# Kernel tuning notes

Measured on AMD Instinct MI355X. Metric: run time of the kernel, lower is better.

The kernel has to match this reference:

```python
import jax, jax.numpy as jnp
import numpy as np

N_NODES = 100000
EMB_DIM = 64
N_EDGES = 1200000
N_LAYERS = 3


def setup_inputs() -> dict:
    key = jax.random.key(0)
    k1, k2, k3 = jax.random.split(key, 3)
    embedding = jax.random.normal(k1, (N_NODES, EMB_DIM), dtype=jnp.float32)
    layer_weights = jnp.ones((N_LAYERS + 1,), dtype=jnp.float32) / (N_LAYERS + 1)
    edge_weight = jax.random.uniform(k2, (N_EDGES,), dtype=jnp.float32)
    edge_index = jax.random.randint(k3, (2, N_EDGES), 0, N_NODES, dtype=jnp.int64)
    return {"embedding": embedding, "layer_weights": layer_weights,
            "edge_weight": edge_weight, "edge_index": edge_index}


def reference(embedding, layer_weights, edge_weight, edge_index):
    # LightGCN inference (dropout off). Each LGConv applies gcn_norm
    # (no self loops) then scatter-adds norm * x[src] into dst.
    n = embedding.shape[0]
    row, col = edge_index[0], edge_index[1]  # source, target

    # gcn_norm: deg over target nodes, symmetric normalization
    deg = jax.ops.segment_sum(edge_weight, col, num_segments=n)
    dinv = jnp.where(deg > 0, jax.lax.rsqrt(deg), 0.0)
    norm = dinv[row] * edge_weight * dinv[col]  # [E]

    x = embedding
    outs = [x]
    for _ in range(N_LAYERS):
        msgs = norm[:, None] * x[row]                         # [E, D] gather
        x = jax.ops.segment_sum(msgs, col, num_segments=n)    # [N, D] scatter
        outs.append(x)

    w = jax.nn.softmax(layer_weights)                         # [L+1]
    comb = jnp.einsum('l,lnd->nd', w, jnp.stack(outs))        # weighted layer combine
    # F.normalize(dim=1), eps=1e-12
    nrm = jnp.maximum(jnp.linalg.norm(comb, axis=1, keepdims=True), 1e-12)
    return comb / nrm
```

## Files before the change

### kernel.cpp

```cpp
#include <hip/hip_runtime.h>

#define N_NODES 100000
#define EMB_DIM 64
#define N_EDGES 1200000

#define BSHIFT  7
#define BNODES  128
#define NBUCKET ((N_NODES + BNODES - 1) / BNODES)
#define CAP     2048
#define EPB     4096
#define NBLK_BIN ((N_EDGES + EPB - 1) / EPB)

#define DBINS 512
#define DNPB  1024
#define NBLK_DEG ((N_NODES + DNPB - 1) / DNPB)

typedef unsigned short ushort8v __attribute__((ext_vector_type(8)));

struct __align__(8) EdgeRec {
    int   s;
    float w;
};

struct __align__(8) BinRec {
    unsigned meta;
    float    ew;
};

__device__ __forceinline__ unsigned short f2bf(float f) {
    unsigned u = __float_as_uint(f);
    u += 0x7FFFu + ((u >> 16) & 1u);
    return (unsigned short)(u >> 16);
}
__device__ __forceinline__ float bf2f(unsigned short h) {
    return __uint_as_float((unsigned)h << 16);
}

__global__ void init_kernel(int* __restrict__ bucket_cursor, int* __restrict__ dhist) {
    int t = threadIdx.x;
    if (t < NBUCKET) bucket_cursor[t] = t * CAP;
    if (t < DBINS)   dhist[t] = 0;
}

__global__ void bin_scatter(const int* __restrict__ row,
                            const int* __restrict__ col,
                            const float* __restrict__ ew,
                            int* __restrict__ bucket_cursor,
                            BinRec* __restrict__ binned) {
    __shared__ int hcnt[NBUCKET];
    __shared__ int hbase[NBUCKET];
    int tid = threadIdx.x;
    if (tid < NBUCKET) hcnt[tid] = 0;
    __syncthreads();
    int base = blockIdx.x * EPB;
    int end = base + EPB; if (end > N_EDGES) end = N_EDGES;
    for (int e = base + tid; e < end; e += 1024)
        atomicAdd(&hcnt[col[e] >> BSHIFT], 1);
    __syncthreads();
    if (tid < NBUCKET) {
        int c = hcnt[tid];
        hbase[tid] = c ? atomicAdd(&bucket_cursor[tid], c) : 0;
        hcnt[tid] = 0;
    }
    __syncthreads();
    for (int e = base + tid; e < end; e += 1024) {
        int c = col[e];
        int b = c >> BSHIFT;
        int rk = atomicAdd(&hcnt[b], 1);
        BinRec r;
        r.meta = (unsigned)row[e] | ((unsigned)(c & (BNODES - 1)) << 20);
        r.ew = ew[e];
        binned[hbase[b] + rk] = r;
    }
}

__global__ void bucket_scan(const int* __restrict__ cursor,
                            int* __restrict__ csr_base,
                            int* __restrict__ start) {
    __shared__ int ws[16];
    int t = threadIdx.x;
    int lane = t & 63, wid = t >> 6;
    int v = (t < NBUCKET) ? (cursor[t] - t * CAP) : 0;
    int inc = v;
    #pragma unroll
    for (int o = 1; o < 64; o <<= 1) {
        int u = __shfl_up(inc, o, 64);
        if (lane >= o) inc += u;
    }
    if (lane == 63) ws[wid] = inc;
    __syncthreads();
    int woff = 0;
    for (int w = 0; w < wid; ++w) woff += ws[w];
    if (t < NBUCKET) csr_base[t] = woff + inc - v;
    if (t == 0) start[N_NODES] = N_EDGES;
}

__global__ void bucket_build(const BinRec* __restrict__ binned,
                             const int* __restrict__ cursor,
                             const int* __restrict__ csr_base,
                             const float* __restrict__ emb,
                             float* __restrict__ dinv,
                             float* __restrict__ rdinv,
                             int* __restrict__ start,
                             EdgeRec* __restrict__ rec,
                             unsigned short* __restrict__ y0,
                             int* __restrict__ dhist) {
    __shared__ int   cnt[BNODES];
    __shared__ float deg[BNODES];
    __shared__ int   cur[BNODES];
    __shared__ int   dh[DBINS];
    __shared__ int   wsum[2];
    int b = blockIdx.x;
    int tid = threadIdx.x;
    if (tid < BNODES) { cnt[tid] = 0; deg[tid] = 0.0f; }
    for (int i = tid; i < DBINS; i += 256) dh[i] = 0;
    __syncthreads();
    int s = b * CAP;
    int n = cursor[b] - s;
    for (int i = tid; i < n; i += 256) {
        BinRec r = binned[s + i];
        int l = r.meta >> 20;
        atomicAdd(&cnt[l], 1);
        atomicAdd(&deg[l], r.ew);
    }
    __syncthreads();
    int lane = tid & 63, wid = tid >> 6;
    int v = (tid < BNODES) ? cnt[tid] : 0;
    int inc = v;
    #pragma unroll
    for (int o = 1; o < 64; o <<= 1) {
        int u = __shfl_up(inc, o, 64);
        if (lane >= o) inc += u;
    }
    if (tid < BNODES && lane == 63) wsum[wid] = inc;
    __syncthreads();
    if (tid < BNODES) {
        int excl = inc - v + ((wid == 1) ? wsum[0] : 0);
        int node = (b << BSHIFT) + tid;
        if (node < N_NODES) {
            int st = csr_base[b] + excl;
            start[node] = st;
            cur[tid] = st;
            float d = deg[tid];
            dinv[node]  = (d > 0.0f) ? rsqrtf(d) : 0.0f;
            rdinv[node] = (d > 0.0f) ? sqrtf(d)  : 0.0f;
            int dd = v; if (dd > DBINS - 1) dd = DBINS - 1;
            atomicAdd(&dh[dd], 1);
        } else {
            cur[tid] = 0;
        }
    }
    __syncthreads();
    for (int i = tid; i < n; i += 256) {
        BinRec r = binned[s + i];
        int l = r.meta >> 20;
        int pos = atomicAdd(&cur[l], 1);
        EdgeRec o;
        o.s = (int)(r.meta & 0xFFFFFu);
        o.w = r.ew;
        rec[pos] = o;
    }
    for (int i = tid; i < DBINS; i += 256)
        if (dh[i]) atomicAdd(&dhist[i], dh[i]);
    #pragma unroll
    for (int pass = 0; pass < 4; ++pass) {
        int g = (pass * 256 + tid) * 8;
        int l = g >> 6;
        int node = (b << BSHIFT) + l;
        if (node < N_NODES) {
            float d = deg[l];
            float dn = (d > 0.0f) ? rsqrtf(d) : 0.0f;
            size_t off = (((size_t)node) << 6) + (g & 63);
            float4 a = *(const float4*)(emb + off);
            float4 bb = *(const float4*)(emb + off + 4);
            uint4 o;
            o.x = (unsigned)f2bf(dn * a.x)  | ((unsigned)f2bf(dn * a.y)  << 16);
            o.y = (unsigned)f2bf(dn * a.z)  | ((unsigned)f2bf(dn * a.w)  << 16);
            o.z = (unsigned)f2bf(dn * bb.x) | ((unsigned)f2bf(dn * bb.y) << 16);
            o.w = (unsigned)f2bf(dn * bb.z) | ((unsigned)f2bf(dn * bb.w) << 16);
            *(uint4*)(y0 + off) = o;
        }
    }
}

__global__ void deg_scan(const int* __restrict__ dhist, int* __restrict__ dcursor) {
    __shared__ int ws[8];
    int t = threadIdx.x;
    int lane = t & 63, wid = t >> 6;
    int v = dhist[t];
    int inc = v;
    #pragma unroll
    for (int o = 1; o < 64; o <<= 1) {
        int u = __shfl_up(inc, o, 64);
        if (lane >= o) inc += u;
    }
    if (lane == 63) ws[wid] = inc;
    __syncthreads();
    int woff = 0;
    for (int w = 0; w < wid; ++w) woff += ws[w];
    dcursor[t] = woff + inc - v;
}

__global__ void deg_scatter(const int* __restrict__ start,
                            int* __restrict__ dcursor,
                            int* __restrict__ perm) {
    __shared__ int h[DBINS];
    __shared__ int hb[DBINS];
    int tid = threadIdx.x;
    for (int i = tid; i < DBINS; i += 256) h[i] = 0;
    __syncthreads();
    int base = blockIdx.x * DNPB;
    int end = base + DNPB; if (end > N_NODES) end = N_NODES;
    for (int n = base + tid; n < end; n += 256) {
        int d = start[n + 1] - start[n];
        if (d > DBINS - 1) d = DBINS - 1;
        atomicAdd(&h[d], 1);
    }
    __syncthreads();
    for (int i = tid; i < DBINS; i += 256) {
        int c = h[i];
        hb[i] = c ? atomicAdd(&dcursor[i], c) : 0;
        h[i] = 0;
    }
    __syncthreads();
    for (int n = base + tid; n < end; n += 256) {
        int d = start[n + 1] - start[n];
        if (d > DBINS - 1) d = DBINS - 1;
        int rk = atomicAdd(&h[d], 1);
        perm[hb[d] + rk] = n;
    }
}

__global__ void prop8_kernel(const unsigned short* __restrict__ yin,
                             unsigned short* __restrict__ yout,
                             const EdgeRec* __restrict__ rec,
                             const int* __restrict__ start,
                             const float* __restrict__ dinv,
                             const int* __restrict__ perm) {
    int t = blockIdx.x * blockDim.x + threadIdx.x;
    int slot = t >> 3;
    int q = (t & 7) << 3;
    if (slot >= N_NODES) return;
    int n = perm[slot];
    int s = start[n], e = start[n + 1];
    float a0 = 0.f, a1 = 0.f, a2 = 0.f, a3 = 0.f;
    float a4 = 0.f, a5 = 0.f, a6 = 0.f, a7 = 0.f;
    int j = s;
    for (; j + 4 <= e; j += 4) {
        EdgeRec r0 = rec[j], r1 = rec[j + 1], r2 = rec[j + 2], r3 = rec[j + 3];
        ushort8v h0 = *(const ushort8v*)(yin + (((size_t)r0.s) << 6) + q);
        ushort8v h1 = *(const ushort8v*)(yin + (((size_t)r1.s) << 6) + q);
        ushort8v h2 = *(const ushort8v*)(yin + (((size_t)r2.s) << 6) + q);
        ushort8v h3 = *(const ushort8v*)(yin + (((size_t)r3.s) << 6) + q);
        a0 += r0.w * bf2f(h0[0]) + r1.w * bf2f(h1[0]) + r2.w * bf2f(h2[0]) + r3.w * bf2f(h3[0]);
        a1 += r0.w * bf2f(h0[1]) + r1.w * bf2f(h1[1]) + r2.w * bf2f(h2[1]) + r3.w * bf2f(h3[1]);
        a2 += r0.w * bf2f(h0[2]) + r1.w * bf2f(h1[2]) + r2.w * bf2f(h2[2]) + r3.w * bf2f(h3[2]);
        a3 += r0.w * bf2f(h0[3]) + r1.w * bf2f(h1[3]) + r2.w * bf2f(h2[3]) + r3.w * bf2f(h3[3]);
        a4 += r0.w * bf2f(h0[4]) + r1.w * bf2f(h1[4]) + r2.w * bf2f(h2[4]) + r3.w * bf2f(h3[4]);
        a5 += r0.w * bf2f(h0[5]) + r1.w * bf2f(h1[5]) + r2.w * bf2f(h2[5]) + r3.w * bf2f(h3[5]);
        a6 += r0.w * bf2f(h0[6]) + r1.w * bf2f(h1[6]) + r2.w * bf2f(h2[6]) + r3.w * bf2f(h3[6]);
        a7 += r0.w * bf2f(h0[7]) + r1.w * bf2f(h1[7]) + r2.w * bf2f(h2[7]) + r3.w * bf2f(h3[7]);
    }
    for (; j < e; ++j) {
        EdgeRec r = rec[j];
        ushort8v h = *(const ushort8v*)(yin + (((size_t)r.s) << 6) + q);
        a0 += r.w * bf2f(h[0]); a1 += r.w * bf2f(h[1]);
        a2 += r.w * bf2f(h[2]); a3 += r.w * bf2f(h[3]);
        a4 += r.w * bf2f(h[4]); a5 += r.w * bf2f(h[5]);
        a6 += r.w * bf2f(h[6]); a7 += r.w * bf2f(h[7]);
    }
    float dn = dinv[n];
    float dn2 = dn * dn;
    uint4 o;
    o.x = (unsigned)f2bf(dn2 * a0) | ((unsigned)f2bf(dn2 * a1) << 16);
    o.y = (unsigned)f2bf(dn2 * a2) | ((unsigned)f2bf(dn2 * a3) << 16);
    o.z = (unsigned)f2bf(dn2 * a4) | ((unsigned)f2bf(dn2 * a5) << 16);
    o.w = (unsigned)f2bf(dn2 * a6) | ((unsigned)f2bf(dn2 * a7) << 16);
    *(uint4*)(yout + (((size_t)n) << 6) + q) = o;
}

__global__ void prop8_combine_kernel(const unsigned short* __restrict__ y2h,
                                     const float* __restrict__ x0,
                                     const unsigned short* __restrict__ y1h,
                                     const EdgeRec* __restrict__ rec,
                                     const int* __restrict__ start,
                                     const float* __restrict__ dinv,
                                     const float* __restrict__ rdinv,
                                     const float* __restrict__ lw,
                                     const int* __restrict__ perm,
                                     float* __restrict__ out) {
    int t = blockIdx.x * blockDim.x + threadIdx.x;
    int slot = t >> 3;
    int q = (t & 7) << 3;
    if (slot >= N_NODES) return;
    int n = perm[slot];
    int s = start[n], e = start[n + 1];
    float a0 = 0.f, a1 = 0.f, a2 = 0.f, a3 = 0.f;
    float a4 = 0.f, a5 = 0.f, a6 = 0.f, a7 = 0.f;
    int j = s;
    for (; j + 4 <= e; j += 4) {
        EdgeRec r0 = rec[j], r1 = rec[j + 1], r2 = rec[j + 2], r3 = rec[j + 3];
        ushort8v h0 = *(const ushort8v*)(y2h + (((size_t)r0.s) << 6) + q);
        ushort8v h1 = *(const ushort8v*)(y2h + (((size_t)r1.s) << 6) + q);
        ushort8v h2 = *(const ushort8v*)(y2h + (((size_t)r2.s) << 6) + q);
        ushort8v h3 = *(const ushort8v*)(y2h + (((size_t)r3.s) << 6) + q);
        a0 += r0.w * bf2f(h0[0]) + r1.w * bf2f(h1[0]) + r2.w * bf2f(h2[0]) + r3.w * bf2f(h3[0]);
        a1 += r0.w * bf2f(h0[1]) + r1.w * bf2f(h1[1]) + r2.w * bf2f(h2[1]) + r3.w * bf2f(h3[1]);
        a2 += r0.w * bf2f(h0[2]) + r1.w * bf2f(h1[2]) + r2.w * bf2f(h2[2]) + r3.w * bf2f(h3[2]);
        a3 += r0.w * bf2f(h0[3]) + r1.w * bf2f(h1[3]) + r2.w * bf2f(h2[3]) + r3.w * bf2f(h3[3]);
        a4 += r0.w * bf2f(h0[4]) + r1.w * bf2f(h1[4]) + r2.w * bf2f(h2[4]) + r3.w * bf2f(h3[4]);
        a5 += r0.w * bf2f(h0[5]) + r1.w * bf2f(h1[5]) + r2.w * bf2f(h2[5]) + r3.w * bf2f(h3[5]);
        a6 += r0.w * bf2f(h0[6]) + r1.w * bf2f(h1[6]) + r2.w * bf2f(h2[6]) + r3.w * bf2f(h3[6]);
        a7 += r0.w * bf2f(h0[7]) + r1.w * bf2f(h1[7]) + r2.w * bf2f(h2[7]) + r3.w * bf2f(h3[7]);
    }
    for (; j < e; ++j) {
        EdgeRec r = rec[j];
        ushort8v h = *(const ushort8v*)(y2h + (((size_t)r.s) << 6) + q);
        a0 += r.w * bf2f(h[0]); a1 += r.w * bf2f(h[1]);
        a2 += r.w * bf2f(h[2]); a3 += r.w * bf2f(h[3]);
        a4 += r.w * bf2f(h[4]); a5 += r.w * bf2f(h[5]);
        a6 += r.w * bf2f(h[6]); a7 += r.w * bf2f(h[7]);
    }
    float dn = dinv[n];
    float rn = rdinv[n];

    float w0 = lw[0], w1 = lw[1], w2 = lw[2], w3 = lw[3];
    float m = fmaxf(fmaxf(w0, w1), fmaxf(w2, w3));
    float e0 = expf(w0 - m), e1 = expf(w1 - m), e2 = expf(w2 - m), e3 = expf(w3 - m);
    float inv_s = 1.0f / (e0 + e1 + e2 + e3);
    float c1 = e1 * rn, c2 = e2 * rn, c3 = e3 * dn;

    size_t off = (((size_t)n) << 6) + q;
    float4 xa = *(const float4*)(x0 + off);
    float4 xb = *(const float4*)(x0 + off + 4);
    ushort8v h1v = *(const ushort8v*)(y1h + off);
    ushort8v h2v = *(const ushort8v*)(y2h + off);

    float v0 = (e0 * xa.x + c1 * bf2f(h1v[0]) + c2 * bf2f(h2v[0]) + c3 * a0) * inv_s;
    float v1 = (e0 * xa.y + c1 * bf2f(h1v[1]) + c2 * bf2f(h2v[1]) + c3 * a1) * inv_s;
    float v2 = (e0 * xa.z + c1 * bf2f(h1v[2]) + c2 * bf2f(h2v[2]) + c3 * a2) * inv_s;
    float v3 = (e0 * xa.w + c1 * bf2f(h1v[3]) + c2 * bf2f(h2v[3]) + c3 * a3) * inv_s;
    float v4 = (e0 * xb.x + c1 * bf2f(h1v[4]) + c2 * bf2f(h2v[4]) + c3 * a4) * inv_s;
    float v5 = (e0 * xb.y + c1 * bf2f(h1v[5]) + c2 * bf2f(h2v[5]) + c3 * a5) * inv_s;
    float v6 = (e0 * xb.z + c1 * bf2f(h1v[6]) + c2 * bf2f(h2v[6]) + c3 * a6) * inv_s;
    float v7 = (e0 * xb.w + c1 * bf2f(h1v[7]) + c2 * bf2f(h2v[7]) + c3 * a7) * inv_s;

    float sq = v0*v0 + v1*v1 + v2*v2 + v3*v3 + v4*v4 + v5*v5 + v6*v6 + v7*v7;
    #pragma unroll
    for (int o = 1; o < 8; o <<= 1) sq += __shfl_xor(sq, o, 64);
    float nrm = fmaxf(sqrtf(sq), 1e-12f);
    float inv_n = 1.0f / nrm;

    float4 oa, ob;
    oa.x = v0 * inv_n; oa.y = v1 * inv_n; oa.z = v2 * inv_n; oa.w = v3 * inv_n;
    ob.x = v4 * inv_n; ob.y = v5 * inv_n; ob.z = v6 * inv_n; ob.w = v7 * inv_n;
    *(float4*)(out + off) = oa;
    *(float4*)(out + off + 4) = ob;
}

extern "C" void kernel_launch(void* const* d_in, const int* in_sizes, int n_in,
                              void* d_out, int out_size, void* d_ws, size_t ws_size,
                              hipStream_t stream) {
    const float* emb = (const float*)d_in[0];
    const float* lw  = (const float*)d_in[1];
    const float* ew  = (const float*)d_in[2];
    const int*   ei  = (const int*)d_in[3];
    const int* row = ei;
    const int* col = ei + N_EDGES;
    float* out = (float*)d_out;

    char* p = (char*)d_ws;
    BinRec*  binned = (BinRec*)p;               p += (size_t)NBUCKET * CAP * sizeof(BinRec);
    EdgeRec* rec    = (EdgeRec*)p;              p += (size_t)N_EDGES * sizeof(EdgeRec);
    unsigned short* y0h = (unsigned short*)p;   p += (size_t)N_NODES * EMB_DIM * 2;
    unsigned short* y1h = (unsigned short*)p;   p += (size_t)N_NODES * EMB_DIM * 2;
    unsigned short* y2h = (unsigned short*)p;   p += (size_t)N_NODES * EMB_DIM * 2;
    float* dinv  = (float*)p;                   p += (size_t)N_NODES * 4;
    float* rdinv = (float*)p;                   p += (size_t)N_NODES * 4;
    int*   startA= (int*)p;                     p += (size_t)(N_NODES + 8) * 4;
    int*   perm  = (int*)p;                     p += (size_t)N_NODES * 4;
    int*   csr_base      = (int*)p;             p += (size_t)NBUCKET * 4;
    int*   bucket_cursor = (int*)p;             p += (size_t)NBUCKET * 4;
    int*   dhist   = (int*)p;                   p += (size_t)DBINS * 4;
    int*   dcursor = (int*)p;                   p += (size_t)DBINS * 4;

    const int B = 256;

    init_kernel<<<1, 1024, 0, stream>>>(bucket_cursor, dhist);
    bin_scatter<<<NBLK_BIN, 1024, 0, stream>>>(row, col, ew, bucket_cursor, binned);
    bucket_scan<<<1, 1024, 0, stream>>>(bucket_cursor, csr_base, startA);
    bucket_build<<<NBUCKET, B, 0, stream>>>(binned, bucket_cursor, csr_base, emb,
                                            dinv, rdinv, startA, rec, y0h, dhist);
    deg_scan<<<1, DBINS, 0, stream>>>(dhist, dcursor);
    deg_scatter<<<NBLK_DEG, B, 0, stream>>>(startA, dcursor, perm);

    long pt = (long)N_NODES * 8;
    int pgrid = (int)((pt + B - 1) / B);
    prop8_kernel<<<pgrid, B, 0, stream>>>(y0h, y1h, rec, startA, dinv, perm);
    prop8_kernel<<<pgrid, B, 0, stream>>>(y1h, y2h, rec, startA, dinv, perm);
    prop8_combine_kernel<<<pgrid, B, 0, stream>>>(y2h, emb, y1h, rec, startA, dinv,
                                                  rdinv, lw, perm, out);
}
```

Measured before the change: 157.1 us.

## Pack edge source and quantized weight into one 32-bit record, unroll gathers by eight

Each edge record now packs the source index (20 bits) with a 15-bit fixed-point weight into 32 bits, replacing the 8-byte int+float struct. This halves edge-stream traffic in the three propagation kernels. The gather loops are unrolled to eight edges so more row loads are in flight. The combine kernel reads layer 0 from the bf16 y0 buffer scaled by the sqrt of the degree instead of the fp32 embedding, falling back to fp32 only for zero-degree nodes. The cost is extra precision loss from the quantized edge weights and from using bf16 for layer 0.

Result: faster. 150.8 us (-4.0%).

```diff
diff --git a/kernel.cpp b/kernel.cpp
--- a/kernel.cpp
+++ b/kernel.cpp
@@ -15,12 +15,10 @@
 #define DNPB  1024
 #define NBLK_DEG ((N_NODES + DNPB - 1) / DNPB)
 
+#define WSCALE 32767.0f
+#define WINV   (1.0f / 32767.0f)
+
 typedef unsigned short ushort8v __attribute__((ext_vector_type(8)));
-
-struct __align__(8) EdgeRec {
-    int   s;
-    float w;
-};
 
 struct __align__(8) BinRec {
     unsigned meta;
@@ -102,7 +100,7 @@
                              float* __restrict__ dinv,
                              float* __restrict__ rdinv,
                              int* __restrict__ start,
-                             EdgeRec* __restrict__ rec,
+                             unsigned* __restrict__ rec,
                              unsigned short* __restrict__ y0,
                              int* __restrict__ dhist) {
     __shared__ int   cnt[BNODES];
@@ -155,10 +153,8 @@
         BinRec r = binned[s + i];
         int l = r.meta >> 20;
         int pos = atomicAdd(&cur[l], 1);
-        EdgeRec o;
-        o.s = (int)(r.meta & 0xFFFFFu);
-        o.w = r.ew;
-        rec[pos] = o;
+        unsigned wq = (unsigned)rintf(r.ew * WSCALE);
+        rec[pos] = ((r.meta & 0xFFFFFu) << 15) | wq;
     }
     for (int i = tid; i < DBINS; i += 256)
         if (dh[i]) atomicAdd(&dhist[i], dh[i]);
@@ -231,9 +227,19 @@
     }
 }
 
+#define DECODE(v, src, w)  { src = (int)((v) >> 15); w = (float)((v) & 0x7FFFu) * WINV; }
+
+#define GATHER_ACC(vv)                                                          \
+    {   int _s; float _w; DECODE(vv, _s, _w);                                   \
+        ushort8v _h = *(const ushort8v*)(yin + (((size_t)_s) << 6) + q);        \
+        a0 += _w * bf2f(_h[0]); a1 += _w * bf2f(_h[1]);                         \
+        a2 += _w * bf2f(_h[2]); a3 += _w * bf2f(_h[3]);                         \
+        a4 += _w * bf2f(_h[4]); a5 += _w * bf2f(_h[5]);                         \
+        a6 += _w * bf2f(_h[6]); a7 += _w * bf2f(_h[7]); }
+
 __global__ void prop8_kernel(const unsigned short* __restrict__ yin,
                              unsigned short* __restrict__ yout,
-                             const EdgeRec* __restrict__ rec,
+                             const unsigned* __restrict__ rec,
                              const int* __restrict__ start,
                              const float* __restrict__ dinv,
                              const int* __restrict__ perm) {
@@ -246,29 +252,59 @@
     float a0 = 0.f, a1 = 0.f, a2 = 0.f, a3 = 0.f;
     float a4 = 0.f, a5 = 0.f, a6 = 0.f, a7 = 0.f;
     int j = s;
-    for (; j + 4 <= e; j += 4) {
-        EdgeRec r0 = rec[j], r1 = rec[j + 1], r2 = rec[j + 2], r3 = rec[j + 3];
-        ushort8v h0 = *(const ushort8v*)(yin + (((size_t)r0.s) << 6) + q);
-        ushort8v h1 = *(const ushort8v*)(yin + (((size_t)r1.s) << 6) + q);
-        ushort8v h2 = *(const ushort8v*)(yin + (((size_t)r2.s) << 6) + q);
-        ushort8v h3 = *(const ushort8v*)(yin + (((size_t)r3.s) << 6) + q);
-        a0 += r0.w * bf2f(h0[0]) + r1.w * bf2f(h1[0]) + r2.w * bf2f(h2[0]) + r3.w * bf2f(h3[0]);
-        a1 += r0.w * bf2f(h0[1]) + r1.w * bf2f(h1[1]) + r2.w * bf2f(h2[1]) + r3.w * bf2f(h3[1]);
-        a2 += r0.w * bf2f(h0[2]) + r1.w * bf2f(h1[2]) + r2.w * bf2f(h2[2]) + r3.w * bf2f(h3[2]);
-        a3 += r0.w * bf2f(h0[3]) + r1.w * bf2f(h1[3]) + r2.w * bf2f(h2[3]) + r3.w * bf2f(h3[3]);
-        a4 += r0.w * bf2f(h0[4]) + r1.w * bf2f(h1[4]) + r2.w * bf2f(h2[4]) + r3.w * bf2f(h3[4]);
-        a5 += r0.w * bf2f(h0[5]) + r1.w * bf2f(h1[5]) + r2.w * bf2f(h2[5]) + r3.w * bf2f(h3[5]);
-        a6 += r0.w * bf2f(h0[6]) + r1.w * bf2f(h1[6]) + r2.w * bf2f(h2[6]) + r3.w * bf2f(h3[6]);
-        a7 += r0.w * bf2f(h0[7]) + r1.w * bf2f(h1[7]) + r2.w * bf2f(h2[7]) + r3.w * bf2f(h3[7]);
-    }
-    for (; j < e; ++j) {
-        EdgeRec r = rec[j];
-        ushort8v h = *(const ushort8v*)(yin + (((size_t)r.s) << 6) + q);
-        a0 += r.w * bf2f(h[0]); a1 += r.w * bf2f(h[1]);
-        a2 += r.w * bf2f(h[2]); a3 += r.w * bf2f(h[3]);
-        a4 += r.w * bf2f(h[4]); a5 += r.w * bf2f(h[5]);
-        a6 += r.w * bf2f(h[6]); a7 += r.w * bf2f(h[7]);
-    }
+    for (; j + 8 <= e; j += 8) {
+        unsigned v0 = rec[j],     v1 = rec[j + 1], v2 = rec[j + 2], v3 = rec[j + 3];
+        unsigned v4 = rec[j + 4], v5 = rec[j + 5], v6 = rec[j + 6], v7 = rec[j + 7];
+        const ushort8v* p0 = (const ushort8v*)(yin + (((size_t)(v0 >> 15)) << 6) + q);
+        const ushort8v* p1 = (const ushort8v*)(yin + (((size_t)(v1 >> 15)) << 6) + q);
+        const ushort8v* p2 = (const ushort8v*)(yin + (((size_t)(v2 >> 15)) << 6) + q);
+        const ushort8v* p3 = (const ushort8v*)(yin + (((size_t)(v3 >> 15)) << 6) + q);
+        const ushort8v* p4 = (const ushort8v*)(yin + (((size_t)(v4 >> 15)) << 6) + q);
+        const ushort8v* p5 = (const ushort8v*)(yin + (((size_t)(v5 >> 15)) << 6) + q);
+        const ushort8v* p6 = (const ushort8v*)(yin + (((size_t)(v6 >> 15)) << 6) + q);
+        const ushort8v* p7 = (const ushort8v*)(yin + (((size_t)(v7 >> 15)) << 6) + q);
+        ushort8v h0 = *p0, h1 = *p1, h2 = *p2, h3 = *p3;
+        ushort8v h4 = *p4, h5 = *p5, h6 = *p6, h7 = *p7;
+        float w0 = (float)(v0 & 0x7FFFu) * WINV, w1 = (float)(v1 & 0x7FFFu) * WINV;
+        float w2 = (float)(v2 & 0x7FFFu) * WINV, w3 = (float)(v3 & 0x7FFFu) * WINV;
+        float w4 = (float)(v4 & 0x7FFFu) * WINV, w5 = (float)(v5 & 0x7FFFu) * WINV;
+        float w6 = (float)(v6 & 0x7FFFu) * WINV, w7 = (float)(v7 & 0x7FFFu) * WINV;
+        a0 += w0*bf2f(h0[0]) + w1*bf2f(h1[0]) + w2*bf2f(h2[0]) + w3*bf2f(h3[0])
+            + w4*bf2f(h4[0]) + w5*bf2f(h5[0]) + w6*bf2f(h6[0]) + w7*bf2f(h7[0]);
+        a1 += w0*bf2f(h0[1]) + w1*bf2f(h1[1]) + w2*bf2f(h2[1]) + w3*bf2f(h3[1])
+            + w4*bf2f(h4[1]) + w5*bf2f(h5[1]) + w6*bf2f(h6[1]) + w7*bf2f(h7[1]);
+        a2 += w0*bf2f(h0[2]) + w1*bf2f(h1[2]) + w2*bf2f(h2[2]) + w3*bf2f(h3[2])
+            + w4*bf2f(h4[2]) + w5*bf2f(h5[2]) + w6*bf2f(h6[2]) + w7*bf2f(h7[2]);
+        a3 += w0*bf2f(h0[3]) + w1*bf2f(h1[3]) + w2*bf2f(h2[3]) + w3*bf2f(h3[3])
+            + w4*bf2f(h4[3]) + w5*bf2f(h5[3]) + w6*bf2f(h6[3]) + w7*bf2f(h7[3]);
+        a4 += w0*bf2f(h0[4]) + w1*bf2f(h1[4]) + w2*bf2f(h2[4]) + w3*bf2f(h3[4])
+            + w4*bf2f(h4[4]) + w5*bf2f(h5[4]) + w6*bf2f(h6[4]) + w7*bf2f(h7[4]);
+        a5 += w0*bf2f(h0[5]) + w1*bf2f(h1[5]) + w2*bf2f(h2[5]) + w3*bf2f(h3[5])
+            + w4*bf2f(h4[5]) + w5*bf2f(h5[5]) + w6*bf2f(h6[5]) + w7*bf2f(h7[5]);
+        a6 += w0*bf2f(h0[6]) + w1*bf2f(h1[6]) + w2*bf2f(h2[6]) + w3*bf2f(h3[6])
+            + w4*bf2f(h4[6]) + w5*bf2f(h5[6]) + w6*bf2f(h6[6]) + w7*bf2f(h7[6]);
+        a7 += w0*bf2f(h0[7]) + w1*bf2f(h1[7]) + w2*bf2f(h2[7]) + w3*bf2f(h3[7])
+            + w4*bf2f(h4[7]) + w5*bf2f(h5[7]) + w6*bf2f(h6[7]) + w7*bf2f(h7[7]);
+    }
+    if (j + 4 <= e) {
+        unsigned v0 = rec[j], v1 = rec[j + 1], v2 = rec[j + 2], v3 = rec[j + 3];
+        ushort8v h0 = *(const ushort8v*)(yin + (((size_t)(v0 >> 15)) << 6) + q);
+        ushort8v h1 = *(const ushort8v*)(yin + (((size_t)(v1 >> 15)) << 6) + q);
+        ushort8v h2 = *(const ushort8v*)(yin + (((size_t)(v2 >> 15)) << 6) + q);
+        ushort8v h3 = *(const ushort8v*)(yin + (((size_t)(v3 >> 15)) << 6) + q);
+        float w0 = (float)(v0 & 0x7FFFu) * WINV, w1 = (float)(v1 & 0x7FFFu) * WINV;
+        float w2 = (float)(v2 & 0x7FFFu) * WINV, w3 = (float)(v3 & 0x7FFFu) * WINV;
+        a0 += w0*bf2f(h0[0]) + w1*bf2f(h1[0]) + w2*bf2f(h2[0]) + w3*bf2f(h3[0]);
+        a1 += w0*bf2f(h0[1]) + w1*bf2f(h1[1]) + w2*bf2f(h2[1]) + w3*bf2f(h3[1]);
+        a2 += w0*bf2f(h0[2]) + w1*bf2f(h1[2]) + w2*bf2f(h2[2]) + w3*bf2f(h3[2]);
+        a3 += w0*bf2f(h0[3]) + w1*bf2f(h1[3]) + w2*bf2f(h2[3]) + w3*bf2f(h3[3]);
+        a4 += w0*bf2f(h0[4]) + w1*bf2f(h1[4]) + w2*bf2f(h2[4]) + w3*bf2f(h3[4]);
+        a5 += w0*bf2f(h0[5]) + w1*bf2f(h1[5]) + w2*bf2f(h2[5]) + w3*bf2f(h3[5]);
+        a6 += w0*bf2f(h0[6]) + w1*bf2f(h1[6]) + w2*bf2f(h2[6]) + w3*bf2f(h3[6]);
+        a7 += w0*bf2f(h0[7]) + w1*bf2f(h1[7]) + w2*bf2f(h2[7]) + w3*bf2f(h3[7]);
+        j += 4;
+    }
+    for (; j < e; ++j) GATHER_ACC(rec[j]);
     float dn = dinv[n];
     float dn2 = dn * dn;
     uint4 o;
@@ -279,10 +315,11 @@
     *(uint4*)(yout + (((size_t)n) << 6) + q) = o;
 }
 
-__global__ void prop8_combine_kernel(const unsigned short* __restrict__ y2h,
-                                     const float* __restrict__ x0,
+__global__ void prop8_combine_kernel(const unsigned short* __restrict__ yin,
+                                     const unsigned short* __restrict__ y0h,
                                      const unsigned short* __restrict__ y1h,
-                                     const EdgeRec* __restrict__ rec,
+                                     const float* __restrict__ emb,
+                                     const unsigned* __restrict__ rec,
                                      const int* __restrict__ start,
                                      const float* __restrict__ dinv,
                                      const float* __restrict__ rdinv,
@@ -298,29 +335,66 @@
     float a0 = 0.f, a1 = 0.f, a2 = 0.f, a3 = 0.f;
     float a4 = 0.f, a5 = 0.f, a6 = 0.f, a7 = 0.f;
     int j = s;
-    for (; j + 4 <= e; j += 4) {
-        EdgeRec r0 = rec[j], r1 = rec[j + 1], r2 = rec[j + 2], r3 = rec[j + 3];
-        ushort8v h0 = *(const ushort8v*)(y2h + (((size_t)r0.s) << 6) + q);
-        ushort8v h1 = *(const ushort8v*)(y2h + (((size_t)r1.s) << 6) + q);
-        ushort8v h2 = *(const ushort8v*)(y2h + (((size_t)r2.s) << 6) + q);
-        ushort8v h3 = *(const ushort8v*)(y2h + (((size_t)r3.s) << 6) + q);
-        a0 += r0.w * bf2f(h0[0]) + r1.w * bf2f(h1[0]) + r2.w * bf2f(h2[0]) + r3.w * bf2f(h3[0]);
-        a1 += r0.w * bf2f(h0[1]) + r1.w * bf2f(h1[1]) + r2.w * bf2f(h2[1]) + r3.w * bf2f(h3[1]);
-        a2 += r0.w * bf2f(h0[2]) + r1.w * bf2f(h1[2]) + r2.w * bf2f(h2[2]) + r3.w * bf2f(h3[2]);
-        a3 += r0.w * bf2f(h0[3]) + r1.w * bf2f(h1[3]) + r2.w * bf2f(h2[3]) + r3.w * bf2f(h3[3]);
-        a4 += r0.w * bf2f(h0[4]) + r1.w * bf2f(h1[4]) + r2.w * bf2f(h2[4]) + r3.w * bf2f(h3[4]);
-        a5 += r0.w * bf2f(h0[5]) + r1.w * bf2f(h1[5]) + r2.w * bf2f(h2[5]) + r3.w * bf2f(h3[5]);
-        a6 += r0.w * bf2f(h0[6]) + r1.w * bf2f(h1[6]) + r2.w * bf2f(h2[6]) + r3.w * bf2f(h3[6]);
-        a7 += r0.w * bf2f(h0[7]) + r1.w * bf2f(h1[7]) + r2.w * bf2f(h2[7]) + r3.w * bf2f(h3[7]);
-    }
-    for (; j < e; ++j) {
-        EdgeRec r = rec[j];
-        ushort8v h = *(const ushort8v*)(y2h + (((size_t)r.s) << 6) + q);
-        a0 += r.w * bf2f(h[0]); a1 += r.w * bf2f(h[1]);
-        a2 += r.w * bf2f(h[2]); a3 += r.w * bf2f(h[3]);
-        a4 += r.w * bf2f(h[4]); a5 += r.w * bf2f(h[5]);
-        a6 += r.w * bf2f(h[6]); a7 += r.w * bf2f(h[7]);
-    }
+    for (; j + 8 <= e; j += 8) {
+        unsigned v0 = rec[j],     v1 = rec[j + 1], v2 = rec[j + 2], v3 = rec[j + 3];
+        unsigned v4 = rec[j + 4], v5 = rec[j + 5], v6 = rec[j + 6], v7 = rec[j + 7];
+        ushort8v h0 = *(const ushort8v*)(yin + (((size_t)(v0 >> 15)) << 6) + q);
+        ushort8v h1 = *(const ushort8v*)(yin + (((size_t)(v1 >> 15)) << 6) + q);
+        ushort8v h2 = *(const ushort8v*)(yin + (((size_t)(v2 >> 15)) << 6) + q);
+        ushort8v h3 = *(const ushort8v*)(yin + (((size_t)(v3 >> 15)) << 6) + q);
+        ushort8v h4 = *(const ushort8v*)(yin + (((size_t)(v4 >> 15)) << 6) + q);
+        ushort8v h5 = *(const ushort8v*)(yin + (((size_t)(v5 >> 15)) << 6) + q);
+        ushort8v h6 = *(const ushort8v*)(yin + (((size_t)(v6 >> 15)) << 6) + q);
+        ushort8v h7 = *(const ushort8v*)(yin + (((size_t)(v7 >> 15)) << 6) + q);
+        float w0 = (float)(v0 & 0x7FFFu) * WINV, w1 = (float)(v1 & 0x7FFFu) * WINV;
+        float w2 = (float)(v2 & 0x7FFFu) * WINV, w3 = (float)(v3 & 0x7FFFu) * WINV;
+        float w4 = (float)(v4 & 0x7FFFu) * WINV, w5 = (float)(v5 & 0x7FFFu) * WINV;
+        float w6 = (float)(v6 & 0x7FFFu) * WINV, w7 = (float)(v7 & 0x7FFFu) * WINV;
+        a0 += w0*bf2f(h0[0]) + w1*bf2f(h1[0]) + w2*bf2f(h2[0]) + w3*bf2f(h3[0])
+            + w4*bf2f(h4[0]) + w5*bf2f(h5[0]) + w6*bf2f(h6[0]) + w7*bf2f(h7[0]);
+        a1 += w0*bf2f(h0[1]) + w1*bf2f(h1[1]) + w2*bf2f(h2[1]) + w3*bf2f(h3[1])
+            + w4*bf2f(h4[1]) + w5*bf2f(h5[1]) + w6*bf2f(h6[1]) + w7*bf2f(h7[1]);
+        a2 += w0*bf2f(h0[2]) + w1*bf2f(h1[2]) + w2*bf2f(h2[2]) + w3*bf2f(h3[2])
+            + w4*bf2f(h4[2]) + w5*bf2f(h5[2]) + w6*bf2f(h6[2]) + w7*bf2f(h7[2]);
+        a3 += w0*bf2f(h0[3]) + w1*bf2f(h1[3]) + w2*bf2f(h2[3]) + w3*bf2f(h3[3])
+            + w4*bf2f(h4[3]) + w5*bf2f(h5[3]) + w6*bf2f(h6[3]) + w7*bf2f(h7[3]);
+        a4 += w0*bf2f(h0[4]) + w1*bf2f(h1[4]) + w2*bf2f(h2[4]) + w3*bf2f(h3[4])
+            + w4*bf2f(h4[4]) + w5*bf2f(h5[4]) + w6*bf2f(h6[4]) + w7*bf2f(h7[4]);
+        a5 += w0*bf2f(h0[5]) + w1*bf2f(h1[5]) + w2*bf2f(h2[5]) + w3*bf2f(h3[5])
+            + w4*bf2f(h4[5]) + w5*bf2f(h5[5]) + w6*bf2f(h6[5]) + w7*bf2f(h7[5]);
+        a6 += w0*bf2f(h0[6]) + w1*bf2f(h1[6]) + w2*bf2f(h2[6]) + w3*bf2f(h3[6])
+            + w4*bf2f(h4[6]) + w5*bf2f(h5[6]) + w6*bf2f(h6[6]) + w7*bf2f(h7[6]);
+        a7 += w0*bf2f(h0[7]) + w1*bf2f(h1[7]) + w2*bf2f(h2[7]) + w3*bf2f(h3[7])
+            + w4*bf2f(h4[7]) + w5*bf2f(h5[7]) + w6*bf2f(h6[7]) + w7*bf2f(h7[7]);
+    }
+    if (j + 4 <= e) {
+        unsigned v0 = rec[j], v1 = rec[j + 1], v2 = rec[j + 2], v3 = rec[j + 3];
+        ushort8v h0 = *(const ushort8v*)(yin + (((size_t)(v0 >> 15)) << 6) + q);
+        ushort8v h1 = *(const ushort8v*)(yin + (((size_t)(v1 >> 15)) << 6) + q);
+        ushort8v h2 = *(const ushort8v*)(yin + (((size_t)(v2 >> 15)) << 6) + q);
+        ushort8v h3 = *(const ushort8v*)(yin + (((size_t)(v3 >> 15)) << 6) + q);
+        float w0 = (float)(v0 & 0x7FFFu) * WINV, w1 = (float)(v1 & 0x7FFFu) * WINV;
+        float w2 = (float)(v2 & 0x7FFFu) * WINV, w3 = (float)(v3 & 0x7FFFu) * WINV;
+        a0 += w0*bf2f(h0[0]) + w1*bf2f(h1[0]) + w2*bf2f(h2[0]) + w3*bf2f(h3[0]);
+        a1 += w0*bf2f(h0[1]) + w1*bf2f(h1[1]) + w2*bf2f(h2[1]) + w3*bf2f(h3[1]);
+        a2 += w0*bf2f(h0[2]) + w1*bf2f(h1[2]) + w2*bf2f(h2[2]) + w3*bf2f(h3[2]);
+        a3 += w0*bf2f(h0[3]) + w1*bf2f(h1[3]) + w2*bf2f(h2[3]) + w3*bf2f(h3[3]);
+        a4 += w0*bf2f(h0[4]) + w1*bf2f(h1[4]) + w2*bf2f(h2[4]) + w3*bf2f(h3[4]);
+        a5 += w0*bf2f(h0[5]) + w1*bf2f(h1[5]) + w2*bf2f(h2[5]) + w3*bf2f(h3[5]);
+        a6 += w0*bf2f(h0[6]) + w1*bf2f(h1[6]) + w2*bf2f(h2[6]) + w3*bf2f(h3[6]);
+        a7 += w0*bf2f(h0[7]) + w1*bf2f(h1[7]) + w2*bf2f(h2[7]) + w3*bf2f(h3[7]);
+        j += 4;
+    }
+    { const unsigned short* yin_ = yin;
+      for (; j < e; ++j) { const unsigned short* yin2 = yin_;
+        unsigned vv = rec[j];
+        int _s = (int)(vv >> 15); float _w = (float)(vv & 0x7FFFu) * WINV;
+        ushort8v _h = *(const ushort8v*)(yin2 + (((size_t)_s) << 6) + q);
+        a0 += _w * bf2f(_h[0]); a1 += _w * bf2f(_h[1]);
+        a2 += _w * bf2f(_h[2]); a3 += _w * bf2f(_h[3]);
+        a4 += _w * bf2f(_h[4]); a5 += _w * bf2f(_h[5]);
+        a6 += _w * bf2f(_h[6]); a7 += _w * bf2f(_h[7]); } }
+
     float dn = dinv[n];
     float rn = rdinv[n];
 
@@ -328,22 +402,29 @@
     float m = fmaxf(fmaxf(w0, w1), fmaxf(w2, w3));
     float e0 = expf(w0 - m), e1 = expf(w1 - m), e2 = expf(w2 - m), e3 = expf(w3 - m);
     float inv_s = 1.0f / (e0 + e1 + e2 + e3);
-    float c1 = e1 * rn, c2 = e2 * rn, c3 = e3 * dn;
+    float c0 = e0 * rn, c1 = e1 * rn, c2 = e2 * rn, c3 = e3 * dn;
 
     size_t off = (((size_t)n) << 6) + q;
-    float4 xa = *(const float4*)(x0 + off);
-    float4 xb = *(const float4*)(x0 + off + 4);
-    ushort8v h1v = *(const ushort8v*)(y1h + off);
-    ushort8v h2v = *(const ushort8v*)(y2h + off);
-
-    float v0 = (e0 * xa.x + c1 * bf2f(h1v[0]) + c2 * bf2f(h2v[0]) + c3 * a0) * inv_s;
-    float v1 = (e0 * xa.y + c1 * bf2f(h1v[1]) + c2 * bf2f(h2v[1]) + c3 * a1) * inv_s;
-    float v2 = (e0 * xa.z + c1 * bf2f(h1v[2]) + c2 * bf2f(h2v[2]) + c3 * a2) * inv_s;
-    float v3 = (e0 * xa.w + c1 * bf2f(h1v[3]) + c2 * bf2f(h2v[3]) + c3 * a3) * inv_s;
-    float v4 = (e0 * xb.x + c1 * bf2f(h1v[4]) + c2 * bf2f(h2v[4]) + c3 * a4) * inv_s;
-    float v5 = (e0 * xb.y + c1 * bf2f(h1v[5]) + c2 * bf2f(h2v[5]) + c3 * a5) * inv_s;
-    float v6 = (e0 * xb.z + c1 * bf2f(h1v[6]) + c2 * bf2f(h2v[6]) + c3 * a6) * inv_s;
-    float v7 = (e0 * xb.w + c1 * bf2f(h1v[7]) + c2 * bf2f(h2v[7]) + c3 * a7) * inv_s;
+    float v0, v1, v2, v3, v4, v5, v6, v7;
+    if (rn != 0.0f) {
+        ushort8v h0v = *(const ushort8v*)(y0h + off);
+        ushort8v h1v = *(const ushort8v*)(y1h + off);
+        ushort8v h2v = *(const ushort8v*)(yin + off);
+        v0 = (c0 * bf2f(h0v[0]) + c1 * bf2f(h1v[0]) + c2 * bf2f(h2v[0]) + c3 * a0) * inv_s;
+        v1 = (c0 * bf2f(h0v[1]) + c1 * bf2f(h1v[1]) + c2 * bf2f(h2v[1]) + c3 * a1) * inv_s;
+        v2 = (c0 * bf2f(h0v[2]) + c1 * bf2f(h1v[2]) + c2 * bf2f(h2v[2]) + c3 * a2) * inv_s;
+        v3 = (c0 * bf2f(h0v[3]) + c1 * bf2f(h1v[3]) + c2 * bf2f(h2v[3]) + c3 * a3) * inv_s;
+        v4 = (c0 * bf2f(h0v[4]) + c1 * bf2f(h1v[4]) + c2 * bf2f(h2v[4]) + c3 * a4) * inv_s;
+        v5 = (c0 * bf2f(h0v[5]) + c1 * bf2f(h1v[5]) + c2 * bf2f(h2v[5]) + c3 * a5) * inv_s;
+        v6 = (c0 * bf2f(h0v[6]) + c1 * bf2f(h1v[6]) + c2 * bf2f(h2v[6]) + c3 * a6) * inv_s;
+        v7 = (c0 * bf2f(h0v[7]) + c1 * bf2f(h1v[7]) + c2 * bf2f(h2v[7]) + c3 * a7) * inv_s;
+    } else {
+        float4 xa = *(const float4*)(emb + off);
+        float4 xb = *(const float4*)(emb + off + 4);
+        float c = e0 * inv_s;
+        v0 = c * xa.x; v1 = c * xa.y; v2 = c * xa.z; v3 = c * xa.w;
+        v4 = c * xb.x; v5 = c * xb.y; v6 = c * xb.z; v7 = c * xb.w;
+    }
 
     float sq = v0*v0 + v1*v1 + v2*v2 + v3*v3 + v4*v4 + v5*v5 + v6*v6 + v7*v7;
     #pragma unroll
@@ -371,7 +452,7 @@
 
     char* p = (char*)d_ws;
     BinRec*  binned = (BinRec*)p;               p += (size_t)NBUCKET * CAP * sizeof(BinRec);
-    EdgeRec* rec    = (EdgeRec*)p;              p += (size_t)N_EDGES * sizeof(EdgeRec);
+    unsigned* rec   = (unsigned*)p;             p += (size_t)N_EDGES * 4;
     unsigned short* y0h = (unsigned short*)p;   p += (size_t)N_NODES * EMB_DIM * 2;
     unsigned short* y1h = (unsigned short*)p;   p += (size_t)N_NODES * EMB_DIM * 2;
     unsigned short* y2h = (unsigned short*)p;   p += (size_t)N_NODES * EMB_DIM * 2;
@@ -398,6 +479,6 @@
     int pgrid = (int)((pt + B - 1) / B);
     prop8_kernel<<<pgrid, B, 0, stream>>>(y0h, y1h, rec, startA, dinv, perm);
     prop8_kernel<<<pgrid, B, 0, stream>>>(y1h, y2h, rec, startA, dinv, perm);
-    prop8_combine_kernel<<<pgrid, B, 0, stream>>>(y2h, emb, y1h, rec, startA, dinv,
-                                                  rdinv, lw, perm, out);
-}
+    prop8_combine_kernel<<<pgrid, B, 0, stream>>>(y2h, y0h, y1h, emb, rec, startA,
+                                                  dinv, rdinv, lw, perm, out);
+}
```
